# Optimization experiments

Measured on AMD Instinct MI355X. Metric: run time of the kernel, lower is better.

## Reference

```python
import jax, jax.numpy as jnp
import numpy as np

B, T, V, E, H, C = 128, 256, 50000, 300, 512, 11
START, STOP = 9, 10
NEG = -100000.0


def _lstm_dir(x, mask, w_ih, w_hh, b_ih, b_hh, reverse):
    # x: [B,T,D]; precompute input-to-gate projection for all timesteps
    gx = jnp.einsum('btd,gd->btg', x, w_ih) + b_ih + b_hh
    m = mask
    if reverse:
        gx = gx[:, ::-1]
        m = m[:, ::-1]
    Bc = x.shape[0]
    Hh = w_hh.shape[1]

    def step(carry, inp):
        h, c = carry
        g, mt = inp
        gates = g + h @ w_hh.T  # [B,4H]
        i, f, gg, o = jnp.split(gates, 4, axis=-1)
        i = jax.nn.sigmoid(i)
        f = jax.nn.sigmoid(f)
        o = jax.nn.sigmoid(o)
        gg = jnp.tanh(gg)
        c_new = f * c + i * gg
        h_new = o * jnp.tanh(c_new)
        mt = mt[:, None]
        h = jnp.where(mt, h_new, h)  # packed-sequence semantics: hold state on pads
        c = jnp.where(mt, c_new, c)
        return (h, c), h

    init = (jnp.zeros((Bc, Hh), x.dtype), jnp.zeros((Bc, Hh), x.dtype))
    _, hs = jax.lax.scan(step, init, (gx.transpose(1, 0, 2), m.T))
    hs = hs.transpose(1, 0, 2)
    if reverse:
        hs = hs[:, ::-1]
    # pad_packed_sequence zeroes padded positions
    return hs * mask[..., None].astype(x.dtype)


def _encode(tokens, mask, embeddings, params):
    x = embeddings[tokens]
    for (wif, whf, bif, bhf, wir, whr, bir, bhr) in params:
        fwd = _lstm_dir(x, mask, wif, whf, bif, bhf, False)
        bwd = _lstm_dir(x, mask, wir, whr, bir, bhr, True)
        x = jnp.concatenate([fwd, bwd], -1)
    return x


def _viterbi(emis, mask, transitions, seq_len):
    def vstep(scores, inp):
        emi, mt = inp
        cand = scores[:, :, None] + transitions[None]  # [B,C,C]
        bt = jnp.argmax(cand, axis=1)
        new = jnp.max(cand, axis=1) + emi
        return jnp.where(mt[:, None], new, scores), bt

    scores0 = jnp.zeros_like(emis[:, 0, :])
    final, backtrack = jax.lax.scan(vstep, scores0, (emis.transpose(1, 0, 2), mask.T))
    final = final + transitions[:, STOP][None]
    best_last = jnp.argmax(final, axis=-1)  # [B]

    ls = jnp.arange(emis.shape[1] - 1, -1, -1)

    def btstep(cur, inp):
        bt_l, l = inp
        emit = jnp.where(l < seq_len, cur, 0)  # pad tail with 0 as in original
        prev = jnp.take_along_axis(bt_l, cur[:, None], axis=1)[:, 0]
        cur = jnp.where((l >= 1) & (l <= seq_len - 1), prev, cur)
        return cur, emit

    _, emits = jax.lax.scan(btstep, best_last, (backtrack[::-1], ls))
    return emits[::-1].T  # [B,T]


def _nll(emis, tags, mask, transitions, seq_len):
    # CRF forward algorithm (replicates original init with -1e5 full scores)
    def fstep(scores, inp):
        emi, mt = inp
        new = jax.nn.logsumexp(scores[:, :, None] + emi[:, None, :] + transitions[None], axis=1)
        return jnp.where(mt[:, None], new, scores), None

    scores0 = jnp.full_like(emis[:, 0, :], NEG)
    final, _ = jax.lax.scan(fstep, scores0, (emis.transpose(1, 0, 2), mask.T))
    fwd_score = jax.nn.logsumexp(final + transitions[:, STOP][None], axis=-1, keepdims=True)

    em_sc = jnp.take_along_axis(emis, tags[..., None], -1)[..., 0]  # [B,T]
    y_aug = jnp.concatenate([jnp.full((tags.shape[0], 1), START, tags.dtype), tags], 1)
    tr_sc = transitions[y_aug[:, :-1], y_aug[:, 1:]]  # [B,T]
    last_tag = jnp.take_along_axis(y_aug, seq_len[:, None], 1)
    last_tr = transitions[last_tag[:, 0], STOP][:, None]
    mf = mask.astype(emis.dtype)
    gold = (mf * (em_sc + tr_sc)).sum(-1, keepdims=True) + last_tr
    return (fwd_score - gold).mean()


def setup_inputs() -> dict:
    key = jax.random.key(0)
    ks = iter(jax.random.split(key, 40))
    sl = jax.random.randint(next(ks), (B,), 1, T + 1)
    sl = -jnp.sort(-sl.at[0].set(T))  # descending, max == T (pack_padded requirement)
    mask = jnp.arange(T)[None, :] < sl[:, None]
    tokens = jax.random.randint(next(ks), (B, T), 0, V)
    tags = jax.random.randint(next(ks), (B, T), 0, 9)
    s = 1.0 / float(np.sqrt(H))

    def u(shape):
        return jax.random.uniform(next(ks), shape, jnp.float32, -s, s)

    inp = dict(tokens=tokens, seq_len=sl, mask=mask, tags=tags,
               embeddings=jax.random.normal(next(ks), (V, E), jnp.float32) * 0.1)
    G = 4 * H
    for li, d in enumerate([E, 2 * H]):
        for suf in ['', 'r']:
            inp[f'w_ih_l{li}{suf}'] = u((G, d))
            inp[f'w_hh_l{li}{suf}'] = u((G, H))
            inp[f'b_ih_l{li}{suf}'] = u((G,))
            inp[f'b_hh_l{li}{suf}'] = u((G,))
    inp['fc_w'] = u((C, 2 * H))
    inp['fc_b'] = u((C,))
    tr = jax.random.normal(next(ks), (C, C), jnp.float32)
    inp['transitions'] = tr.at[START, :].set(-1.0).at[:, STOP].set(-1.0)
    return inp


def reference(tokens, seq_len, mask, tags, embeddings,
              w_ih_l0, w_hh_l0, b_ih_l0, b_hh_l0,
              w_ih_l0r, w_hh_l0r, b_ih_l0r, b_hh_l0r,
              w_ih_l1, w_hh_l1, b_ih_l1, b_hh_l1,
              w_ih_l1r, w_hh_l1r, b_ih_l1r, b_hh_l1r,
              fc_w, fc_b, transitions):
    params = [(w_ih_l0, w_hh_l0, b_ih_l0, b_hh_l0, w_ih_l0r, w_hh_l0r, b_ih_l0r, b_hh_l0r),
              (w_ih_l1, w_hh_l1, b_ih_l1, b_hh_l1, w_ih_l1r, w_hh_l1r, b_ih_l1r, b_hh_l1r)]
    out = _encode(tokens, mask, embeddings, params)  # [B,T,2H]
    emis = jnp.einsum('bth,ch->btc', out, fc_w) + fc_b  # CRF fc (dropout=eval no-op)
    pred = _viterbi(emis, mask, transitions, seq_len)
    loss = _nll(emis, tags, mask, transitions, seq_len)
    return pred, loss
```

## Files before the change

### kernel.cpp

```cpp
#include <hip/hip_runtime.h>
#include <hip/hip_bf16.h>
#include <hip/hip_fp16.h>

#define BB   128
#define TT   256
#define EE   300
#define KP0  320
#define HH   512
#define GG   2048
#define NC   11
#define MM   (BB*TT)
#define START_TAG 9
#define STOP_TAG  10
#define NEGV (-100000.0f)

typedef _Float16 h2_t __attribute__((ext_vector_type(2)));
typedef _Float16 h4_t __attribute__((ext_vector_type(4)));
typedef _Float16 h8_t __attribute__((ext_vector_type(8)));
typedef float    f4_t __attribute__((ext_vector_type(4)));

__device__ __forceinline__ float sigf(float x) {
    return __builtin_amdgcn_rcpf(1.0f + __expf(-x));
}
__device__ __forceinline__ float tanh_fast(float x) {
    float e = __expf(2.0f * x);
    return 1.0f - 2.0f * __builtin_amdgcn_rcpf(e + 1.0f);
}

__device__ __forceinline__ void gload_lds16(const void* g, void* l) {
    __builtin_amdgcn_global_load_lds(
        (const __attribute__((address_space(1))) void*)(unsigned long long)(uintptr_t)g,
        (__attribute__((address_space(3))) void*)(unsigned int)(uintptr_t)l,
        16, 0, 0);
}

__global__ __launch_bounds__(256) void prep_kernel(float* out, int* flags,
                                                   const float* __restrict__ wi0,  _Float16* __restrict__ o0,
                                                   const float* __restrict__ wi0r, _Float16* __restrict__ o0r,
                                                   const float* __restrict__ wi1,  _Float16* __restrict__ o1,
                                                   const float* __restrict__ wi1r, _Float16* __restrict__ o1r) {
    const int b = blockIdx.x, tid = threadIdx.x;
    if (b == 0) {
        if (tid == 0) out[MM] = 0.0f;
        for (int i = tid; i < 1024; i += 256) flags[i] = 0;
    }
    const float* src; _Float16* dst; int K, Kp4, base;
    if (b < 640)       { src = wi0;  dst = o0;  K = EE;   Kp4 = 80;  base = 0; }
    else if (b < 1280) { src = wi0r; dst = o0r; K = EE;   Kp4 = 80;  base = 640; }
    else if (b < 3328) { src = wi1;  dst = o1;  K = 1024; Kp4 = 256; base = 1280; }
    else               { src = wi1r; dst = o1r; K = 1024; Kp4 = 256; base = 3328; }
    int idx = (b - base) * 256 + tid;
    int r = idx / Kp4, c4 = idx % Kp4, c = c4 * 4;
    h4_t v;
    if (c < K) {
        float4 f = *(const float4*)(src + (size_t)r * K + c);
        v[0] = (_Float16)f.x; v[1] = (_Float16)f.y; v[2] = (_Float16)f.z; v[3] = (_Float16)f.w;
    } else {
        v[0] = v[1] = v[2] = v[3] = (_Float16)0.0f;
    }
    *(h4_t*)(dst + (size_t)r * (Kp4 * 4) + c) = v;
}

__global__ __launch_bounds__(256) void embed16_kernel(const int* __restrict__ tok,
                                                      const float* __restrict__ emb,
                                                      _Float16* __restrict__ x0,
                                                      int total4) {
    int idx = blockIdx.x * 256 + threadIdx.x;
    if (idx >= total4) return;
    int m = idx / (KP0 / 4), c4 = idx % (KP0 / 4), c = c4 * 4;
    h4_t v;
    if (c < EE) {
        float4 f = *(const float4*)(emb + (size_t)tok[m] * EE + c);
        v[0] = (_Float16)f.x; v[1] = (_Float16)f.y; v[2] = (_Float16)f.z; v[3] = (_Float16)f.w;
    } else {
        v[0] = v[1] = v[2] = v[3] = (_Float16)0.0f;
    }
    *(h4_t*)(x0 + (size_t)m * KP0 + c) = v;
}

__global__ __launch_bounds__(256) void gemm_bt_kernel(const _Float16* __restrict__ A,
                                                      const _Float16* __restrict__ Wf,
                                                      const float* __restrict__ b1,
                                                      const float* __restrict__ b2,
                                                      _Float16* __restrict__ C,
                                                      int Kp) {
    __shared__ __align__(16) char smem[36864];
    _Float16* As = (_Float16*)smem;
    _Float16* Bs = (_Float16*)(smem + 16384);
    const int tid = threadIdx.x;
    const int m0 = blockIdx.y * 128, n0 = blockIdx.x * 128;
    const int wv = tid >> 6, lane = tid & 63;
    const int wm = wv & 1, wn = wv >> 1;
    const int col = lane & 15, quad = lane >> 4;
    const int rb = lane >> 3;
    const int cb = (lane & 7) * 8;

    f4_t acc[4][4];
#pragma unroll
    for (int i = 0; i < 4; ++i)
#pragma unroll
        for (int j = 0; j < 4; ++j) acc[i][j] = (f4_t){0.f, 0.f, 0.f, 0.f};

    for (int k0 = 0; k0 < Kp; k0 += 64) {
#pragma unroll
        for (int c = 0; c < 4; ++c) {
            int slab = c * 32 + wv * 8;
            gload_lds16(A  + (size_t)(m0 + slab + rb) * Kp + k0 + cb, As + slab * 64);
            gload_lds16(Wf + (size_t)(n0 + slab + rb) * Kp + k0 + cb, Bs + slab * 64);
        }
        __syncthreads();
#pragma unroll
        for (int kk = 0; kk < 2; ++kk) {
            h8_t af[4], bf[4];
#pragma unroll
            for (int i = 0; i < 4; ++i) {
                af[i] = *(const h8_t*)(As + (wm * 64 + i * 16 + col) * 64 + kk * 32 + quad * 8);
                bf[i] = *(const h8_t*)(Bs + (wn * 64 + i * 16 + col) * 64 + kk * 32 + quad * 8);
            }
#pragma unroll
            for (int mi = 0; mi < 4; ++mi)
#pragma unroll
                for (int ni = 0; ni < 4; ++ni)
                    acc[mi][ni] = __builtin_amdgcn_mfma_f32_16x16x32_f16(af[mi], bf[ni], acc[mi][ni], 0, 0, 0);
        }
        __syncthreads();
    }

    _Float16* Ct = (_Float16*)smem;
#pragma unroll
    for (int ni = 0; ni < 4; ++ni) {
        int n = n0 + wn * 64 + ni * 16 + col;
        float bias = b1[n] + b2[n];
#pragma unroll
        for (int mi = 0; mi < 4; ++mi) {
#pragma unroll
            for (int r = 0; r < 4; ++r) {
                int mrow = wm * 64 + mi * 16 + quad * 4 + r;
                Ct[mrow * 136 + wn * 64 + ni * 16 + col] = (_Float16)(acc[mi][ni][r] + bias);
            }
        }
    }
    __syncthreads();
    {
        int row = tid >> 1, half = tid & 1;
#pragma unroll
        for (int cc2 = 0; cc2 < 8; ++cc2) {
            h8_t v = *(const h8_t*)(Ct + row * 136 + half * 64 + cc2 * 8);
            *(h8_t*)(C + (size_t)(m0 + row) * GG + n0 + half * 64 + cc2 * 8) = v;
        }
    }
}

__global__ __launch_bounds__(256, 1) void lstm_rec3_kernel(
        const _Float16* __restrict__ gx_f, const _Float16* __restrict__ gx_r,
        const float* __restrict__ whh_f, const float* __restrict__ whh_r,
        const int* __restrict__ seqlen, int c0, int nbg,
        _Float16* __restrict__ hs, _Float16* __restrict__ hbuf, int* __restrict__ flags) {
    extern __shared__ _Float16 Wlds[];
    _Float16* hstage = Wlds + 32768;

    const int wg = blockIdx.x;
    const int gs = wg & 15;
    const int grp = wg >> 4;
    const int bg = grp % nbg;
    const int dir = grp / nbg;
    const _Float16* gx = dir ? gx_r : gx_f;
    const float* W = dir ? whh_r : whh_f;
    int* myFlags = flags + grp * 16;
    _Float16* hb = hbuf + (size_t)grp * 2 * 16384;

    const int tid = threadIdx.x;
    const int wv = tid >> 6, lane = tid & 63;
    const int mt = wv & 1;
    const int p  = wv >> 1;
    const int col = lane & 15, quad = lane >> 4;

    for (int e = tid; e < 4096; e += 256) {
        int ln = e & 63, kc = (e >> 6) & 15, nt = e >> 10;
        int pp = nt >> 1;
        int n_in_pair = ((nt & 1) << 4) + (ln & 15);
        int gt = n_in_pair >> 3, jj = n_in_pair & 7;
        int R = gt * 512 + gs * 16 + pp * 8 + jj;
        int k = kc * 32 + (ln >> 4) * 8;
        const float4* src = (const float4*)(W + (size_t)R * 512 + k);
        float4 f0 = src[0], f1 = src[1];
        h8_t v;
        v[0] = (_Float16)f0.x; v[1] = (_Float16)f0.y; v[2] = (_Float16)f0.z; v[3] = (_Float16)f0.w;
        v[4] = (_Float16)f1.x; v[5] = (_Float16)f1.y; v[6] = (_Float16)f1.z; v[7] = (_Float16)f1.w;
        *(h8_t*)(Wlds + (size_t)e * 8) = v;
    }
    __syncthreads();

    h8_t Bf0[16], Bf1[16];
#pragma unroll
    for (int kc = 0; kc < 16; ++kc) {
        Bf0[kc] = *(const h8_t*)(Wlds + (((p * 2 + 0) * 16 + kc) * 64 + lane) * 8);
        Bf1[kc] = *(const h8_t*)(Wlds + (((p * 2 + 1) * 16 + kc) * 64 + lane) * 8);
    }

    const int maxsl = seqlen[c0 + bg * 32];
    int sl_r[4];
#pragma unroll
    for (int r = 0; r < 4; ++r) sl_r[r] = seqlen[c0 + bg * 32 + mt * 16 + quad * 4 + r];

    const int jglob = gs * 16 + p * 8 + (col & 7);
    const int hi = col >> 3;

    _Float16 pg0[4], pg1[4];
#pragma unroll
    for (int r = 0; r < 4; ++r) {
        pg0[r] = (_Float16)0.0f; pg1[r] = (_Float16)0.0f;
        if (0 < sl_r[r]) {
            int tm = dir ? (sl_r[r] - 1) : 0;
            int b_loc = bg * 32 + mt * 16 + quad * 4 + r;
            size_t base = ((size_t)(b_loc * TT + tm)) * GG;
            pg0[r] = gx[base + hi * 512 + jglob];
            pg1[r] = gx[base + 1024 + hi * 512 + jglob];
        }
    }

    if (tid < 64) {
        int m = tid >> 1, half = tid & 1;
        h8_t z = {};
        const _Float16* dst = hb + 16384 + m * 512 + gs * 16 + half * 8;
        asm volatile("global_store_dwordx4 %0, %1, off sc0 sc1" :: "v"(dst), "v"(z) : "memory");
        asm volatile("s_waitcnt vmcnt(0)" ::: "memory");
        if (tid == 0) {
            int one = 1;
            asm volatile("global_store_dword %0, %1, off sc0 sc1" :: "v"(myFlags + gs), "v"(one) : "memory");
        }
    }

    float cst[4] = {0.f, 0.f, 0.f, 0.f};
    float hst[4] = {0.f, 0.f, 0.f, 0.f};

    for (int s = 0; s < maxsl; ++s) {
        if (tid < 16) {
            const int* fp = myFlags + tid;
            int v, it = 0;
            for (;;) {
                asm volatile("global_load_dword %0, %1, off sc0 sc1\n\ts_waitcnt vmcnt(0)"
                             : "=v"(v) : "v"(fp) : "memory");
                if (v >= s + 1) break;
                if (it >= 8) __builtin_amdgcn_s_sleep(2);
                ++it;
            }
        }
        __syncthreads();

        const _Float16* hrd = hb + ((s + 1) & 1) * 16384;
        _Float16* hwr = hb + (s & 1) * 16384;

        h8_t a[16];
        const _Float16* ap = hrd + (mt * 16 + col) * 512 + quad * 8;
#pragma unroll
        for (int kc = 0; kc < 16; ++kc)
            asm volatile("global_load_dwordx4 %0, %1, off sc0 sc1"
                         : "=v"(a[kc]) : "v"(ap + kc * 32));
        asm volatile("s_waitcnt vmcnt(0)" ::: "memory");
        __builtin_amdgcn_sched_barrier(0);

        f4_t acc0a = {0.f, 0.f, 0.f, 0.f}, acc0b = {0.f, 0.f, 0.f, 0.f};
        f4_t acc1a = {0.f, 0.f, 0.f, 0.f}, acc1b = {0.f, 0.f, 0.f, 0.f};
#pragma unroll
        for (int kc = 0; kc < 8; ++kc) {
            acc0a = __builtin_amdgcn_mfma_f32_16x16x32_f16(a[kc], Bf0[kc], acc0a, 0, 0, 0);
            acc1a = __builtin_amdgcn_mfma_f32_16x16x32_f16(a[kc], Bf1[kc], acc1a, 0, 0, 0);
        }
#pragma unroll
        for (int kc = 8; kc < 16; ++kc) {
            acc0b = __builtin_amdgcn_mfma_f32_16x16x32_f16(a[kc], Bf0[kc], acc0b, 0, 0, 0);
            acc1b = __builtin_amdgcn_mfma_f32_16x16x32_f16(a[kc], Bf1[kc], acc1b, 0, 0, 0);
        }
        f4_t acc0 = acc0a + acc0b;
        f4_t acc1 = acc1a + acc1b;

#pragma unroll
        for (int r = 0; r < 4; ++r) {
            const bool valid = (s < sl_r[r]);
            float a0 = acc0[r] + (float)pg0[r];
            float a1 = acc1[r] + (float)pg1[r];
            float x0v = __shfl_xor(a0, 8);
            float x1v = __shfl_xor(a1, 8);
            float gi = hi ? x0v : a0;
            float gf = hi ? a0 : x0v;
            float gg2 = hi ? x1v : a1;
            float go = hi ? a1 : x1v;
            if (valid) {
                float cn = sigf(gf) * cst[r] + sigf(gi) * tanh_fast(gg2);
                cst[r] = cn;
                hst[r] = sigf(go) * tanh_fast(cn);
            }
            if (!hi)
                hstage[(mt * 16 + quad * 4 + r) * 16 + p * 8 + (col & 7)] = (_Float16)hst[r];
        }
        __syncthreads();

        if (tid < 64) {
            int m = tid >> 1, half = tid & 1;
            h8_t v = *(const h8_t*)(hstage + m * 16 + half * 8);
            const _Float16* dst = hwr + m * 512 + gs * 16 + half * 8;
            asm volatile("global_store_dwordx4 %0, %1, off sc0 sc1" :: "v"(dst), "v"(v) : "memory");
            asm volatile("s_waitcnt vmcnt(0)" ::: "memory");
            if (tid == 0) {
                int fv = s + 2;
                asm volatile("global_store_dword %0, %1, off sc0 sc1" :: "v"(myFlags + gs), "v"(fv) : "memory");
            }
        }

#pragma unroll
        for (int r = 0; r < 4; ++r) {
            const bool valid = (s < sl_r[r]);
            if (valid && !hi) {
                int b_loc = bg * 32 + mt * 16 + quad * 4 + r;
                int tm = dir ? (sl_r[r] - 1 - s) : s;
                hs[((size_t)(b_loc * TT + tm) << 10) + (dir << 9) + jglob] = (_Float16)hst[r];
            }
        }
        {
            int sn = s + 1;
#pragma unroll
            for (int r = 0; r < 4; ++r) {
                pg0[r] = (_Float16)0.0f; pg1[r] = (_Float16)0.0f;
                if (sn < sl_r[r]) {
                    int tm = dir ? (sl_r[r] - 1 - sn) : sn;
                    int b_loc = bg * 32 + mt * 16 + quad * 4 + r;
                    size_t base = ((size_t)(b_loc * TT + tm)) * GG;
                    pg0[r] = gx[base + hi * 512 + jglob];
                    pg1[r] = gx[base + 1024 + hi * 512 + jglob];
                }
            }
        }
    }
}

__global__ __launch_bounds__(256) void emis_kernel(const _Float16* __restrict__ hs,
                                                   const float* __restrict__ fc_w,
                                                   const float* __restrict__ fc_b,
                                                   float* __restrict__ emis, int Mc) {
    __shared__ __align__(16) float Wl[NC * 1024];
    __shared__ float fb[NC];
    const int tid = threadIdx.x;
    {
        const float4* s4 = (const float4*)fc_w;
        float4* d4 = (float4*)Wl;
        for (int i = tid; i < NC * 256; i += 256) d4[i] = s4[i];
        if (tid < NC) fb[tid] = fc_b[tid];
    }
    __syncthreads();
    const int wv = tid >> 6, lane = tid & 63;

    for (int i = 0; i < 4; ++i) {
        int m = blockIdx.x * 16 + wv * 4 + i;
        if (m >= Mc) return;
        const h8_t* xp = (const h8_t*)(hs + (size_t)m * 1024);
        h8_t xa = xp[lane * 2], xb = xp[lane * 2 + 1];
        float xf[16];
#pragma unroll
        for (int j = 0; j < 8; ++j) { xf[j] = (float)xa[j]; xf[8 + j] = (float)xb[j]; }

        float s[NC];
#pragma unroll
        for (int c = 0; c < NC; ++c) {
            const float4* wr = (const float4*)(Wl + c * 1024 + lane * 16);
            float4 w0 = wr[0], w1 = wr[1], w2 = wr[2], w3 = wr[3];
            s[c] = xf[0] * w0.x + xf[1] * w0.y + xf[2] * w0.z + xf[3] * w0.w
                 + xf[4] * w1.x + xf[5] * w1.y + xf[6] * w1.z + xf[7] * w1.w
                 + xf[8] * w2.x + xf[9] * w2.y + xf[10] * w2.z + xf[11] * w2.w
                 + xf[12] * w3.x + xf[13] * w3.y + xf[14] * w3.z + xf[15] * w3.w;
        }
#pragma unroll
        for (int off = 32; off > 0; off >>= 1)
#pragma unroll
            for (int c = 0; c < NC; ++c) s[c] += __shfl_down(s[c], off);
        if (lane == 0) {
            float* eo = emis + (size_t)m * NC;
#pragma unroll
            for (int c = 0; c < NC; ++c) eo[c] = s[c] + fb[c];
        }
    }
}

__global__ __launch_bounds__(64) void crf_kernel(const float* __restrict__ emis,
                                                 const int* __restrict__ seq_len,
                                                 const int* __restrict__ tags,
                                                 const float* __restrict__ trans,
                                                 float* __restrict__ out, int c0) {
    const int b_loc = blockIdx.x;
    const int b = c0 + b_loc;
    const int lane = threadIdx.x;
    __shared__ float tr[NC * NC];
    __shared__ unsigned char btl[TT * NC];
    for (int i = lane; i < NC * NC; i += 64) tr[i] = trans[i];
    __syncthreads();
    const int sl = seq_len[b];
    const bool act = lane < NC;
    const int jj = act ? lane : 0;

    float vs = 0.0f;
    float ns = NEGV;

    float ej_cur = act ? emis[(size_t)(b_loc * TT) * NC + lane] : 0.0f;
    for (int t = 0; t < sl; ++t) {
        float ej_next = (act && t + 1 < sl) ? emis[(size_t)(b_loc * TT + t + 1) * NC + lane] : 0.0f;
        float vmax = -1e30f, nmax = -1e30f;
        int varg = 0;
        float nsave[NC];
#pragma unroll
        for (int i = 0; i < NC; ++i) {
            float vi = __shfl(vs, i);
            float ni = __shfl(ns, i);
            float tij = tr[i * NC + jj];
            float cv = vi + tij;
            if (cv > vmax) { vmax = cv; varg = i; }
            float cn = ni + tij;
            nsave[i] = cn;
            if (cn > nmax) nmax = cn;
        }
        float ssum = 0.f;
#pragma unroll
        for (int i = 0; i < NC; ++i) ssum += expf(nsave[i] - nmax);
        if (act) {
            vs = vmax + ej_cur;
            ns = nmax + logf(ssum) + ej_cur;
            btl[t * NC + lane] = (unsigned char)varg;
        }
        ej_cur = ej_next;
    }

    float finv = act ? vs + tr[lane * NC + STOP_TAG] : -1e30f;
    float finn = act ? ns + tr[lane * NC + STOP_TAG] : -1e30f;
    float vbest = -1e30f, fmax = -1e30f;
    int barg = 0;
#pragma unroll
    for (int j = 0; j < NC; ++j) {
        float v = __shfl(finv, j);
        if (v > vbest) { vbest = v; barg = j; }
        float n = __shfl(finn, j);
        if (n > fmax) fmax = n;
    }
    float fsum = 0.f;
#pragma unroll
    for (int j = 0; j < NC; ++j) fsum += expf(__shfl(finn, j) - fmax);
    float fwd = fmax + logf(fsum);

    float gsum = 0.f;
    for (int t = lane; t < sl; t += 64) {
        int tg = tags[b * TT + t];
        int pv = (t == 0) ? START_TAG : tags[b * TT + t - 1];
        gsum += emis[(size_t)(b_loc * TT + t) * NC + tg] + tr[pv * NC + tg];
    }
#pragma unroll
    for (int off = 32; off > 0; off >>= 1) gsum += __shfl_down(gsum, off);

    if (lane == 0) {
        float gold = gsum + tr[tags[b * TT + sl - 1] * NC + STOP_TAG];
        atomicAdd(out + MM, (fwd - gold) * (1.0f / (float)BB));
        int cur = barg;
        for (int l = sl - 1; l >= 0; --l) {
            out[b * TT + l] = (float)cur;
            if (l >= 1) cur = (int)btl[l * NC + cur];
        }
    }
    for (int l = sl + lane; l < TT; l += 64) out[b * TT + l] = 0.0f;
}

extern "C" void kernel_launch(void* const* d_in, const int* in_sizes, int n_in,
                              void* d_out, int out_size, void* d_ws, size_t ws_size,
                              hipStream_t stream) {
    (void)in_sizes; (void)n_in; (void)out_size;
    const int* tokens = (const int*)d_in[0];
    const int* seqlen = (const int*)d_in[1];
    const int* tags = (const int*)d_in[3];
    const float* emb = (const float*)d_in[4];
    const float* w_ih_l0  = (const float*)d_in[5];
    const float* w_hh_l0  = (const float*)d_in[6];
    const float* b_ih_l0  = (const float*)d_in[7];
    const float* b_hh_l0  = (const float*)d_in[8];
    const float* w_ih_l0r = (const float*)d_in[9];
    const float* w_hh_l0r = (const float*)d_in[10];
    const float* b_ih_l0r = (const float*)d_in[11];
    const float* b_hh_l0r = (const float*)d_in[12];
    const float* w_ih_l1  = (const float*)d_in[13];
    const float* w_hh_l1  = (const float*)d_in[14];
    const float* b_ih_l1  = (const float*)d_in[15];
    const float* b_hh_l1  = (const float*)d_in[16];
    const float* w_ih_l1r = (const float*)d_in[17];
    const float* w_hh_l1r = (const float*)d_in[18];
    const float* b_ih_l1r = (const float*)d_in[19];
    const float* b_hh_l1r = (const float*)d_in[20];
    const float* fc_w  = (const float*)d_in[21];
    const float* fc_b  = (const float*)d_in[22];
    const float* trans = (const float*)d_in[23];

    const size_t per_b = 2097152u + 524288u + 163840u + 11264u + 2816u;
    const size_t fixed = 524288u + 4096u + 2u * 1310720u + 2u * 4194304u;
    int Bc = 128;
    while (Bc > 32 && fixed + per_b * (size_t)Bc > ws_size) Bc >>= 1;

    char* ws = (char*)d_ws;
    _Float16* hbuf = (_Float16*)ws;
    int* flags = (int*)(ws + 524288u);
    _Float16* w0f = (_Float16*)(ws + 528384u);
    _Float16* w0r = (_Float16*)(ws + 528384u + 1310720u);
    _Float16* w1f = (_Float16*)(ws + 528384u + 2u * 1310720u);
    _Float16* w1r = (_Float16*)(ws + 528384u + 2u * 1310720u + 4194304u);
    char* p = ws + fixed;
    _Float16* gxf   = (_Float16*)p;   p += (size_t)Bc * 1048576u;
    _Float16* gxr   = (_Float16*)p;   p += (size_t)Bc * 1048576u;
    _Float16* hs    = (_Float16*)p;   p += (size_t)Bc * 524288u;
    _Float16* x0f16 = (_Float16*)p;   p += (size_t)Bc * 163840u;
    float* emis     = (float*)p;      p += (size_t)Bc * 11264u;
    float* out = (float*)d_out;

    prep_kernel<<<5376, 256, 0, stream>>>(out, flags,
                                          w_ih_l0, w0f, w_ih_l0r, w0r,
                                          w_ih_l1, w1f, w_ih_l1r, w1r);

    const int nbg = Bc / 32;
    const int nchunk = BB / Bc;
    for (int cidx = 0; cidx < nchunk; ++cidx) {
        const int c0 = cidx * Bc;
        const int Mc = Bc * TT;
        dim3 gdim(GG / 128, Mc / 128);
        int* fl_l0 = flags + (cidx * 2 + 0) * 128;
        int* fl_l1 = flags + (cidx * 2 + 1) * 128;

        embed16_kernel<<<(Mc * 80 + 255) / 256, 256, 0, stream>>>(tokens + c0 * TT, emb, x0f16, Mc * 80);
        gemm_bt_kernel<<<gdim, 256, 0, stream>>>(x0f16, w0f, b_ih_l0,  b_hh_l0,  gxf, KP0);
        gemm_bt_kernel<<<gdim, 256, 0, stream>>>(x0f16, w0r, b_ih_l0r, b_hh_l0r, gxr, KP0);
        lstm_rec3_kernel<<<2 * nbg * 16, 256, 66560, stream>>>(
            gxf, gxr, w_hh_l0, w_hh_l0r, seqlen, c0, nbg, hs, hbuf, fl_l0);
        gemm_bt_kernel<<<gdim, 256, 0, stream>>>(hs, w1f, b_ih_l1,  b_hh_l1,  gxf, 1024);
        gemm_bt_kernel<<<gdim, 256, 0, stream>>>(hs, w1r, b_ih_l1r, b_hh_l1r, gxr, 1024);
        lstm_rec3_kernel<<<2 * nbg * 16, 256, 66560, stream>>>(
            gxf, gxr, w_hh_l1, w_hh_l1r, seqlen, c0, nbg, hs, hbuf, fl_l1);
        emis_kernel<<<Mc / 16, 256, 0, stream>>>(hs, fc_w, fc_b, emis, Mc);
        crf_kernel<<<Bc, 64, 0, stream>>>(emis, seqlen, tags, trans, out, c0);
    }
}
```

Baseline: 5.049 ms.

## Double-buffer GEMM LDS tiles with XOR swizzle and retune spin-wait sleeps

The input-projection GEMM now uses two LDS buffers, so the next K-tile's global-to-LDS loads are issued before the current tile's MFMAs. Waits use partial vmcnt and raw s_barrier instead of __syncthreads. The global column chunk is XOR-swizzled by row, and the fragment reads undo it, to reduce LDS bank conflicts. LDS use grows from 36 to 64 KB, which can lower occupancy. Separately, the recurrent flag spin-loop now sleeps from the first poll (short sleeps at first, longer later), which may add latency on the serial critical path.

```diff
diff --git a/kernel.cpp b/kernel.cpp
--- a/kernel.cpp
+++ b/kernel.cpp
@@ -84,16 +84,19 @@
                                                       const float* __restrict__ b2,
                                                       _Float16* __restrict__ C,
                                                       int Kp) {
-    __shared__ __align__(16) char smem[36864];
-    _Float16* As = (_Float16*)smem;
-    _Float16* Bs = (_Float16*)(smem + 16384);
+    __shared__ __align__(16) char smem[65536];
+    _Float16* As0 = (_Float16*)smem;
+    _Float16* Bs0 = (_Float16*)(smem + 16384);
+    _Float16* As1 = (_Float16*)(smem + 32768);
+    _Float16* Bs1 = (_Float16*)(smem + 49152);
     const int tid = threadIdx.x;
     const int m0 = blockIdx.y * 128, n0 = blockIdx.x * 128;
     const int wv = tid >> 6, lane = tid & 63;
     const int wm = wv & 1, wn = wv >> 1;
     const int col = lane & 15, quad = lane >> 4;
     const int rb = lane >> 3;
-    const int cb = (lane & 7) * 8;
+    const int cbs = ((lane & 7) * 8) ^ (rb << 3);
+    const int rsw = (lane & 7) * 8;
 
     f4_t acc[4][4];
 #pragma unroll
@@ -101,21 +104,38 @@
 #pragma unroll
         for (int j = 0; j < 4; ++j) acc[i][j] = (f4_t){0.f, 0.f, 0.f, 0.f};
 
-    for (int k0 = 0; k0 < Kp; k0 += 64) {
-#pragma unroll
-        for (int c = 0; c < 4; ++c) {
-            int slab = c * 32 + wv * 8;
-            gload_lds16(A  + (size_t)(m0 + slab + rb) * Kp + k0 + cb, As + slab * 64);
-            gload_lds16(Wf + (size_t)(n0 + slab + rb) * Kp + k0 + cb, Bs + slab * 64);
-        }
-        __syncthreads();
+#define STAGE(Ad, Bd, kk0)                                                              \
+    _Pragma("unroll")                                                                   \
+    for (int c = 0; c < 4; ++c) {                                                       \
+        int slab = c * 32 + wv * 8;                                                     \
+        gload_lds16(A  + (size_t)(m0 + slab + rb) * Kp + (kk0) + cbs, (Ad) + slab * 64);\
+        gload_lds16(Wf + (size_t)(n0 + slab + rb) * Kp + (kk0) + cbs, (Bd) + slab * 64);\
+    }
+
+    const int nt = Kp >> 6;
+    STAGE(As0, Bs0, 0);
+
+    for (int t = 0; t < nt; ++t) {
+        const _Float16* Ac = (t & 1) ? As1 : As0;
+        const _Float16* Bc = (t & 1) ? Bs1 : Bs0;
+        if (t + 1 < nt) {
+            _Float16* An = (t & 1) ? As0 : As1;
+            _Float16* Bn = (t & 1) ? Bs0 : Bs1;
+            STAGE(An, Bn, (t + 1) * 64);
+            asm volatile("s_waitcnt vmcnt(8)" ::: "memory");
+        } else {
+            asm volatile("s_waitcnt vmcnt(0)" ::: "memory");
+        }
+        __builtin_amdgcn_s_barrier();
+        __builtin_amdgcn_sched_barrier(0);
+
 #pragma unroll
         for (int kk = 0; kk < 2; ++kk) {
             h8_t af[4], bf[4];
 #pragma unroll
             for (int i = 0; i < 4; ++i) {
-                af[i] = *(const h8_t*)(As + (wm * 64 + i * 16 + col) * 64 + kk * 32 + quad * 8);
-                bf[i] = *(const h8_t*)(Bs + (wn * 64 + i * 16 + col) * 64 + kk * 32 + quad * 8);
+                af[i] = *(const h8_t*)(Ac + (wm * 64 + i * 16 + col) * 64 + ((kk * 32 + quad * 8) ^ rsw));
+                bf[i] = *(const h8_t*)(Bc + (wn * 64 + i * 16 + col) * 64 + ((kk * 32 + quad * 8) ^ rsw));
             }
 #pragma unroll
             for (int mi = 0; mi < 4; ++mi)
@@ -123,8 +143,10 @@
                 for (int ni = 0; ni < 4; ++ni)
                     acc[mi][ni] = __builtin_amdgcn_mfma_f32_16x16x32_f16(af[mi], bf[ni], acc[mi][ni], 0, 0, 0);
         }
-        __syncthreads();
-    }
+        __builtin_amdgcn_sched_barrier(0);
+        __builtin_amdgcn_s_barrier();
+    }
+#undef STAGE
 
     _Float16* Ct = (_Float16*)smem;
 #pragma unroll
@@ -242,7 +264,8 @@
                 asm volatile("global_load_dword %0, %1, off sc0 sc1\n\ts_waitcnt vmcnt(0)"
                              : "=v"(v) : "v"(fp) : "memory");
                 if (v >= s + 1) break;
-                if (it >= 8) __builtin_amdgcn_s_sleep(2);
+                if (it < 3) __builtin_amdgcn_s_sleep(1);
+                else        __builtin_amdgcn_s_sleep(4);
                 ++it;
             }
         }
```

New measurement: 4.828 ms. -4.4%, faster.
